# Performance work log

Hardware: AMD Instinct MI355X
Metric: run time of the kernel (lower is better)

The kernel has to match this reference:

```python
import jax, jax.numpy as jnp
import numpy as np

ID, IH, IW = 8, 16, 16
HEADS, DIM_HEAD = 8, 32
INP, OUP = 256, 256
B = 4
N = ID * IH * IW  # 2048
INNER = HEADS * DIM_HEAD  # 256
SCALE = DIM_HEAD ** -0.5


def _make_relative_pos():
    # Faithful to the torch ctor: 3D coords, pairwise diffs, linearize, shift to >=0
    z, y, x = np.meshgrid(np.arange(ID), np.arange(IH), np.arange(IW), indexing='ij')
    coords = np.stack([z.ravel(), y.ravel(), x.ravel()], axis=1)  # [N,3]
    rel = coords[:, None, :] - coords[None, :, :]                 # [N,N,3]
    rp = rel[:, :, 0] * (IH * IW) + rel[:, :, 1] * IW + rel[:, :, 2]
    rp = rp - rp.min()
    return jnp.asarray(rp, dtype=jnp.int32)                       # [N,N]


def setup_inputs() -> dict:
    key = jax.random.key(0)
    k1, k2, k3, k4, k5 = jax.random.split(key, 5)
    table_size = ID * IH * IW * 8  # 16384, as in nn.Embedding ctor
    return {
        "x": jax.random.normal(k1, (B, N, INP), dtype=jnp.float32),
        "w_qkv": jax.random.normal(k2, (INP, 3 * INNER), dtype=jnp.float32) * (INP ** -0.5),
        "bias_table": jax.random.normal(k3, (table_size, 1), dtype=jnp.float32),
        "w_out": jax.random.normal(k4, (INNER, OUP), dtype=jnp.float32) * (INNER ** -0.5),
        "b_out": jax.random.normal(k5, (OUP,), dtype=jnp.float32),
        "relative_pos": _make_relative_pos(),
    }


def reference(x, w_qkv, bias_table, w_out, b_out, relative_pos):
    Bb, Nn, C = x.shape
    qkv = x @ w_qkv                                   # [B, N, 3*H*D]
    qkv = qkv.reshape(Bb, Nn, 3, HEADS, DIM_HEAD)
    qkv = jnp.transpose(qkv, (2, 0, 3, 1, 4))         # [3, B, H, N, D]
    q, k, v = qkv[0], qkv[1], qkv[2]
    q = q * SCALE
    attn = jnp.einsum('bhnd,bhmd->bhnm', q, k)        # [B, H, N, N]
    bias = bias_table[relative_pos, 0]                # [N, N], shared across B,H
    attn = attn + bias
    attn = jax.nn.softmax(attn, axis=-1)
    out = jnp.einsum('bhnm,bhmd->bhnd', attn, v)      # [B, H, N, D]
    out = jnp.transpose(out, (0, 2, 1, 3)).reshape(Bb, Nn, INNER)
    return out @ w_out + b_out                        # dropout p=0 -> identity
```

## Files before the change

kernel.cpp:

```cpp
#include <hip/hip_runtime.h>

typedef unsigned short u16;
typedef unsigned int u32;
typedef __attribute__((ext_vector_type(8))) short bf16x8;
typedef __attribute__((ext_vector_type(4))) float f32x4;

#define MFMA16(a, b, c) __builtin_amdgcn_mfma_f32_16x16x32_bf16(a, b, c, 0, 0, 0)

__device__ __forceinline__ u16 f2bf(float f) {
    union { float f; u32 i; } v; v.f = f;
    u32 x = v.i;
    return (u16)((x + 0x7FFFu + ((x >> 16) & 1u)) >> 16);
}
__device__ __forceinline__ bf16x8 cvt8(const float* __restrict__ p) {
    float4 a = *(const float4*)p;
    float4 b = *(const float4*)(p + 4);
    bf16x8 r;
    r[0] = (short)f2bf(a.x); r[1] = (short)f2bf(a.y);
    r[2] = (short)f2bf(a.z); r[3] = (short)f2bf(a.w);
    r[4] = (short)f2bf(b.x); r[5] = (short)f2bf(b.y);
    r[6] = (short)f2bf(b.z); r[7] = (short)f2bf(b.w);
    return r;
}

__global__ __launch_bounds__(256) void k_transpose(const float* __restrict__ wqkv,
                                                   const float* __restrict__ wout,
                                                   u16* __restrict__ wqkvT,
                                                   u16* __restrict__ woutT) {
    int idx = blockIdx.x * 256 + threadIdx.x;
    if (idx < 768 * 256) {
        int n = idx >> 8, k = idx & 255;
        wqkvT[idx] = f2bf(wqkv[k * 768 + n]);
    }
    if (idx < 256 * 256) {
        int n = idx >> 8, k = idx & 255;
        woutT[idx] = f2bf(wout[k * 256 + n]);
    }
}

__global__ __launch_bounds__(256) void k_gemm_qkv(const float* __restrict__ x,
                                                  const u16* __restrict__ wT,
                                                  u16* __restrict__ qkv) {
    const int tid = threadIdx.x;
    const int wave = tid >> 6, lane = tid & 63, quad = lane >> 4, ql = lane & 15;
    const int mbase = blockIdx.x * 128 + (wave & 1) * 64;
    const int nbase = blockIdx.y * 64 + (wave >> 1) * 32;
    const float QSCALE = 0.17677669529663687f;
    f32x4 acc[4][2];
#pragma unroll
    for (int i = 0; i < 4; ++i)
#pragma unroll
        for (int j = 0; j < 2; ++j) acc[i][j] = (f32x4){0.f, 0.f, 0.f, 0.f};
#pragma unroll
    for (int ks = 0; ks < 8; ++ks) {
        bf16x8 af[4], bfm[2];
#pragma unroll
        for (int ms = 0; ms < 4; ++ms)
            af[ms] = cvt8(x + (size_t)(mbase + ms * 16 + ql) * 256 + ks * 32 + quad * 8);
#pragma unroll
        for (int ns = 0; ns < 2; ++ns)
            bfm[ns] = *(const bf16x8*)(wT + (size_t)(nbase + ns * 16 + ql) * 256 + ks * 32 + quad * 8);
#pragma unroll
        for (int ms = 0; ms < 4; ++ms)
#pragma unroll
            for (int ns = 0; ns < 2; ++ns)
                acc[ms][ns] = MFMA16(af[ms], bfm[ns], acc[ms][ns]);
    }
#pragma unroll
    for (int ms = 0; ms < 4; ++ms)
#pragma unroll
        for (int ns = 0; ns < 2; ++ns) {
            int colb = nbase + ns * 16;
            int t = colb >> 8;
            int Mrow0 = mbase + ms * 16 + quad * 4;
            int bb = Mrow0 >> 11, nn0 = Mrow0 & 2047;
            int col = colb + ql;
            int h = (col & 255) >> 5, d = col & 31;
            if (t == 2) {
                u16 e0 = f2bf(acc[ms][ns][0]), e1 = f2bf(acc[ms][ns][1]);
                u16 e2 = f2bf(acc[ms][ns][2]), e3 = f2bf(acc[ms][ns][3]);
                uint2 pp; pp.x = e0 | ((u32)e1 << 16); pp.y = e2 | ((u32)e3 << 16);
                *(uint2*)(qkv + (size_t)2 * 2097152 + (size_t)(bb * 8 + h) * 65536 +
                          (size_t)d * 2048 + nn0) = pp;
            } else {
                float sc = (t == 0) ? QSCALE : 1.0f;
#pragma unroll
                for (int r = 0; r < 4; ++r)
                    qkv[(size_t)t * 2097152 + ((size_t)(bb * 8 + h) * 2048 + nn0 + r) * 32 + d] =
                        f2bf(acc[ms][ns][r] * sc);
            }
        }
}

__global__ __launch_bounds__(256) void k_attn(const u16* __restrict__ q,
                                              const u16* __restrict__ k,
                                              const u16* __restrict__ vT,
                                              const float* __restrict__ table,
                                              u16* __restrict__ att) {
    __shared__ float tblf[4096];
    __shared__ u32 pT[4][1280];
    const int tid = threadIdx.x;
    const int bh = blockIdx.x & 31, qt = blockIdx.x >> 5;
    const int wave = tid >> 6, lane = tid & 63, quad = lane >> 4, ql = lane & 15;

    for (int i = tid; i < 1024; i += 256)
        ((float4*)tblf)[i] = ((const float4*)table)[i];
    __syncthreads();

    const u16* kbh = k + (size_t)bh * 65536;
    const u16* vbh = vT + (size_t)bh * 65536;
    const int qr0 = qt * 128 + wave * 32 + ql;
    bf16x8 qf[2];
    qf[0] = *(const bf16x8*)(q + ((size_t)bh * 2048 + qr0) * 32 + quad * 8);
    qf[1] = *(const bf16x8*)(q + ((size_t)bh * 2048 + qr0 + 16) * 32 + quad * 8);
    const int base0 = qr0 + 2047 - quad * 4;

    f32x4 oT[2][2], lacc[2];
#pragma unroll
    for (int a = 0; a < 2; ++a) {
        lacc[a] = (f32x4){0.f, 0.f, 0.f, 0.f};
#pragma unroll
        for (int b = 0; b < 2; ++b) oT[a][b] = (f32x4){0.f, 0.f, 0.f, 0.f};
    }
    u32* pw = &pT[wave][0];

#define LOADK(KF, VF, KT) do {                                                          \
    _Pragma("unroll") for (int j_ = 0; j_ < 4; ++j_)                                    \
        KF[j_] = *(const bf16x8*)(kbh + (size_t)((KT) * 64 + j_ * 16 + ql) * 32 + quad * 8); \
    _Pragma("unroll") for (int f_ = 0; f_ < 4; ++f_) {                                  \
        int c_ = f_ >> 1, dt_ = f_ & 1;                                                 \
        VF[f_] = *(const bf16x8*)(vbh + (size_t)(dt_ * 16 + ql) * 2048 +                \
                                  (KT) * 64 + c_ * 32 + quad * 8); }                    \
} while (0)

#define BODY(KF, VF, KT) do {                                                           \
    _Pragma("unroll") for (int qh = 0; qh < 2; ++qh) {                                  \
        f32x4 z_ = {0.f, 0.f, 0.f, 0.f};                                                \
        f32x4 s_[4];                                                                    \
        _Pragma("unroll") for (int j_ = 0; j_ < 4; ++j_)                                \
            s_[j_] = MFMA16(KF[j_], qf[qh], z_);                                        \
        _Pragma("unroll") for (int j_ = 0; j_ < 4; ++j_) {                              \
            _Pragma("unroll") for (int r_ = 0; r_ < 4; ++r_) {                          \
                float sv_ = s_[j_][r_] +                                                \
                    tblf[base0 + qh * 16 - (KT) * 64 - j_ * 16 - r_];                   \
                s_[j_][r_] = __expf(sv_);                                               \
            }                                                                           \
            lacc[qh] += s_[j_];                                                         \
        }                                                                               \
        _Pragma("unroll") for (int j_ = 0; j_ < 4; ++j_)                                \
            _Pragma("unroll") for (int p_ = 0; p_ < 2; ++p_) {                          \
                u32 lo_ = __float_as_uint(s_[j_][2 * p_]) >> 16;                        \
                u32 hi_ = __float_as_uint(s_[j_][2 * p_ + 1]) & 0xFFFF0000u;            \
                pw[(qh * 32 + j_ * 8 + quad * 2 + p_) * 20 + ql] = hi_ | lo_;           \
            }                                                                           \
        _Pragma("unroll") for (int c_ = 0; c_ < 2; ++c_) {                              \
            union { u32 u[4]; bf16x8 v; } bb_;                                          \
            _Pragma("unroll") for (int kk_ = 0; kk_ < 4; ++kk_)                         \
                bb_.u[kk_] = pw[(qh * 32 + c_ * 16 + quad * 4 + kk_) * 20 + ql];        \
            oT[qh][0] = MFMA16(VF[c_ * 2 + 0], bb_.v, oT[qh][0]);                       \
            oT[qh][1] = MFMA16(VF[c_ * 2 + 1], bb_.v, oT[qh][1]);                       \
        }                                                                               \
    }                                                                                   \
} while (0)

    bf16x8 kf0[4], vf0[4], kf1[4], vf1[4];
    LOADK(kf0, vf0, 0);
    for (int kt2 = 0; kt2 < 16; ++kt2) {
        int ktA = 2 * kt2, ktB = 2 * kt2 + 1;
        int ktC = (kt2 == 15) ? 31 : (2 * kt2 + 2);
        LOADK(kf1, vf1, ktB);
        BODY(kf0, vf0, ktA);
        LOADK(kf0, vf0, ktC);
        BODY(kf1, vf1, ktB);
    }
#undef LOADK
#undef BODY

#pragma unroll
    for (int qh = 0; qh < 2; ++qh) {
        float l = lacc[qh][0] + lacc[qh][1] + lacc[qh][2] + lacc[qh][3];
        l += __shfl_xor(l, 16);
        l += __shfl_xor(l, 32);
        float inv = 1.0f / l;
        size_t base = ((size_t)bh * 2048 + qr0 + qh * 16) * 32;
#pragma unroll
        for (int dt = 0; dt < 2; ++dt) {
            u16 e0 = f2bf(oT[qh][dt][0] * inv), e1 = f2bf(oT[qh][dt][1] * inv);
            u16 e2 = f2bf(oT[qh][dt][2] * inv), e3 = f2bf(oT[qh][dt][3] * inv);
            uint2 pp; pp.x = e0 | ((u32)e1 << 16); pp.y = e2 | ((u32)e3 << 16);
            *(uint2*)(att + base + dt * 16 + quad * 4) = pp;
        }
    }
}

__global__ __launch_bounds__(256) void k_gemm_out(const u16* __restrict__ attq,
                                                  const u16* __restrict__ wT,
                                                  const float* __restrict__ bout,
                                                  float* __restrict__ out) {
    const int tid = threadIdx.x;
    const int wave = tid >> 6, lane = tid & 63, quad = lane >> 4, ql = lane & 15;
    const int mbase = blockIdx.x * 128 + (wave & 1) * 64;
    const int nbase = blockIdx.y * 64 + (wave >> 1) * 32;
    f32x4 acc[4][2];
#pragma unroll
    for (int i = 0; i < 4; ++i)
#pragma unroll
        for (int j = 0; j < 2; ++j) acc[i][j] = (f32x4){0.f, 0.f, 0.f, 0.f};
#pragma unroll
    for (int ks = 0; ks < 8; ++ks) {
        bf16x8 af[4], bfm[2];
#pragma unroll
        for (int ms = 0; ms < 4; ++ms) {
            int row = mbase + ms * 16 + ql;
            af[ms] = *(const bf16x8*)(attq +
                ((size_t)((row >> 11) * 8 + ks) * 2048 + (row & 2047)) * 32 + quad * 8);
        }
#pragma unroll
        for (int ns = 0; ns < 2; ++ns)
            bfm[ns] = *(const bf16x8*)(wT + (size_t)(nbase + ns * 16 + ql) * 256 + ks * 32 + quad * 8);
#pragma unroll
        for (int ms = 0; ms < 4; ++ms)
#pragma unroll
            for (int ns = 0; ns < 2; ++ns)
                acc[ms][ns] = MFMA16(af[ms], bfm[ns], acc[ms][ns]);
    }
#pragma unroll
    for (int ms = 0; ms < 4; ++ms)
#pragma unroll
        for (int ns = 0; ns < 2; ++ns)
#pragma unroll
            for (int r = 0; r < 4; ++r) {
                int Mrow = mbase + ms * 16 + quad * 4 + r;
                int col = nbase + ns * 16 + ql;
                out[(size_t)Mrow * 256 + col] = acc[ms][ns][r] + bout[col];
            }
}

extern "C" void kernel_launch(void* const* d_in, const int* in_sizes, int n_in,
                              void* d_out, int out_size, void* d_ws, size_t ws_size,
                              hipStream_t stream) {
    const float* x    = (const float*)d_in[0];
    const float* wqkv = (const float*)d_in[1];
    const float* btab = (const float*)d_in[2];
    const float* wout = (const float*)d_in[3];
    const float* bout = (const float*)d_in[4];
    float* out = (float*)d_out;

    if (ws_size < (size_t)13107200) return;
    u16* ws = (u16*)d_ws;
    u16* wqkvT = ws;
    u16* woutT = wqkvT + 196608;
    u16* qkv   = woutT + 65536;

    hipLaunchKernelGGL(k_transpose, dim3(768), dim3(256), 0, stream, wqkv, wout, wqkvT, woutT);
    hipLaunchKernelGGL(k_gemm_qkv, dim3(64, 12), dim3(256), 0, stream, x, wqkvT, qkv);
    hipLaunchKernelGGL(k_attn, dim3(512), dim3(256), 0, stream,
                       qkv, qkv + 2097152, qkv + 2 * 2097152, btab, qkv);
    hipLaunchKernelGGL(k_gemm_out, dim3(64, 4), dim3(256), 0, stream, qkv, woutT, bout, out);
}
```

Measured before the change: 164.3 us.

## Prep bf16 inputs, fold log2e into scale, shrink attention tiles, MFMA row sums

A single prep kernel now converts x to bf16 (staged in the output buffer) and transposes both weights, folding scale*log2e into the Q weight columns. The QKV GEMM therefore reads bf16 directly and skips per-element scaling. Attention tiles are halved to 64 queries per block (1024 blocks), giving each wave one 16-row Q tile. Each block loads only the slice of the bias table it needs, pre-multiplied by log2e, and uses hardware exp2. Row sums come from an MFMA against a ones vector instead of VALU accumulation and shuffles, and bf16 packing uses a perm instruction. The trade-off is that K/V loads are amortized over fewer queries.

```diff
diff --git a/kernel.cpp b/kernel.cpp
--- a/kernel.cpp
+++ b/kernel.cpp
@@ -7,45 +7,51 @@
 
 #define MFMA16(a, b, c) __builtin_amdgcn_mfma_f32_16x16x32_bf16(a, b, c, 0, 0, 0)
 
+__device__ __forceinline__ float hw_exp2(float x) { return __builtin_amdgcn_exp2f(x); }
+
 __device__ __forceinline__ u16 f2bf(float f) {
     union { float f; u32 i; } v; v.f = f;
     u32 x = v.i;
     return (u16)((x + 0x7FFFu + ((x >> 16) & 1u)) >> 16);
 }
-__device__ __forceinline__ bf16x8 cvt8(const float* __restrict__ p) {
-    float4 a = *(const float4*)p;
-    float4 b = *(const float4*)(p + 4);
-    bf16x8 r;
-    r[0] = (short)f2bf(a.x); r[1] = (short)f2bf(a.y);
-    r[2] = (short)f2bf(a.z); r[3] = (short)f2bf(a.w);
-    r[4] = (short)f2bf(b.x); r[5] = (short)f2bf(b.y);
-    r[6] = (short)f2bf(b.z); r[7] = (short)f2bf(b.w);
-    return r;
-}
-
-__global__ __launch_bounds__(256) void k_transpose(const float* __restrict__ wqkv,
-                                                   const float* __restrict__ wout,
-                                                   u16* __restrict__ wqkvT,
-                                                   u16* __restrict__ woutT) {
-    int idx = blockIdx.x * 256 + threadIdx.x;
-    if (idx < 768 * 256) {
-        int n = idx >> 8, k = idx & 255;
-        wqkvT[idx] = f2bf(wqkv[k * 768 + n]);
-    }
-    if (idx < 256 * 256) {
-        int n = idx >> 8, k = idx & 255;
-        woutT[idx] = f2bf(wout[k * 256 + n]);
-    }
-}
-
-__global__ __launch_bounds__(256) void k_gemm_qkv(const float* __restrict__ x,
+
+__global__ __launch_bounds__(256) void k_prep(const float* __restrict__ x,
+                                              const float* __restrict__ wqkv,
+                                              const float* __restrict__ wout,
+                                              u16* __restrict__ xb,
+                                              u16* __restrict__ wqkvT,
+                                              u16* __restrict__ woutT) {
+    const float QSCALE2 = 0.2550566756538019f;
+    int bx = blockIdx.x, tid = threadIdx.x;
+    if (bx < 1024) {
+        int base = bx * 2048 + tid * 8;
+        float4 a = *(const float4*)(x + base);
+        float4 b = *(const float4*)(x + base + 4);
+        uint4 r;
+        r.x = f2bf(a.x) | ((u32)f2bf(a.y) << 16);
+        r.y = f2bf(a.z) | ((u32)f2bf(a.w) << 16);
+        r.z = f2bf(b.x) | ((u32)f2bf(b.y) << 16);
+        r.w = f2bf(b.z) | ((u32)f2bf(b.w) << 16);
+        *(uint4*)(xb + base) = r;
+    } else if (bx < 1792) {
+        int idx = (bx - 1024) * 256 + tid;
+        int n = idx >> 8, kk = idx & 255;
+        float sc = (n < 256) ? QSCALE2 : 1.0f;
+        wqkvT[idx] = f2bf(wqkv[kk * 768 + n] * sc);
+    } else {
+        int idx = (bx - 1792) * 256 + tid;
+        int n = idx >> 8, kk = idx & 255;
+        woutT[idx] = f2bf(wout[kk * 256 + n]);
+    }
+}
+
+__global__ __launch_bounds__(256) void k_gemm_qkv(const u16* __restrict__ xb,
                                                   const u16* __restrict__ wT,
                                                   u16* __restrict__ qkv) {
     const int tid = threadIdx.x;
     const int wave = tid >> 6, lane = tid & 63, quad = lane >> 4, ql = lane & 15;
     const int mbase = blockIdx.x * 128 + (wave & 1) * 64;
     const int nbase = blockIdx.y * 64 + (wave >> 1) * 32;
-    const float QSCALE = 0.17677669529663687f;
     f32x4 acc[4][2];
 #pragma unroll
     for (int i = 0; i < 4; ++i)
@@ -56,7 +62,7 @@
         bf16x8 af[4], bfm[2];
 #pragma unroll
         for (int ms = 0; ms < 4; ++ms)
-            af[ms] = cvt8(x + (size_t)(mbase + ms * 16 + ql) * 256 + ks * 32 + quad * 8);
+            af[ms] = *(const bf16x8*)(xb + (size_t)(mbase + ms * 16 + ql) * 256 + ks * 32 + quad * 8);
 #pragma unroll
         for (int ns = 0; ns < 2; ++ns)
             bfm[ns] = *(const bf16x8*)(wT + (size_t)(nbase + ns * 16 + ql) * 256 + ks * 32 + quad * 8);
@@ -83,11 +89,10 @@
                 *(uint2*)(qkv + (size_t)2 * 2097152 + (size_t)(bb * 8 + h) * 65536 +
                           (size_t)d * 2048 + nn0) = pp;
             } else {
-                float sc = (t == 0) ? QSCALE : 1.0f;
 #pragma unroll
                 for (int r = 0; r < 4; ++r)
                     qkv[(size_t)t * 2097152 + ((size_t)(bb * 8 + h) * 2048 + nn0 + r) * 32 + d] =
-                        f2bf(acc[ms][ns][r] * sc);
+                        f2bf(acc[ms][ns][r]);
             }
         }
 }
@@ -97,31 +102,32 @@
                                               const u16* __restrict__ vT,
                                               const float* __restrict__ table,
                                               u16* __restrict__ att) {
-    __shared__ float tblf[4096];
-    __shared__ u32 pT[4][1280];
+    __shared__ float tbl2[2112];
+    __shared__ u32 pT[4][640];
     const int tid = threadIdx.x;
     const int bh = blockIdx.x & 31, qt = blockIdx.x >> 5;
     const int wave = tid >> 6, lane = tid & 63, quad = lane >> 4, ql = lane & 15;
-
-    for (int i = tid; i < 1024; i += 256)
-        ((float4*)tblf)[i] = ((const float4*)table)[i];
+    const float LOG2E = 1.4426950408889634f;
+
+    const float4* tg = (const float4*)(table + qt * 64);
+    for (int i = tid; i < 528; i += 256) {
+        float4 t = tg[i];
+        t.x *= LOG2E; t.y *= LOG2E; t.z *= LOG2E; t.w *= LOG2E;
+        ((float4*)tbl2)[i] = t;
+    }
     __syncthreads();
 
     const u16* kbh = k + (size_t)bh * 65536;
     const u16* vbh = vT + (size_t)bh * 65536;
-    const int qr0 = qt * 128 + wave * 32 + ql;
-    bf16x8 qf[2];
-    qf[0] = *(const bf16x8*)(q + ((size_t)bh * 2048 + qr0) * 32 + quad * 8);
-    qf[1] = *(const bf16x8*)(q + ((size_t)bh * 2048 + qr0 + 16) * 32 + quad * 8);
-    const int base0 = qr0 + 2047 - quad * 4;
-
-    f32x4 oT[2][2], lacc[2];
-#pragma unroll
-    for (int a = 0; a < 2; ++a) {
-        lacc[a] = (f32x4){0.f, 0.f, 0.f, 0.f};
-#pragma unroll
-        for (int b = 0; b < 2; ++b) oT[a][b] = (f32x4){0.f, 0.f, 0.f, 0.f};
-    }
+    const int qr0 = qt * 64 + wave * 16 + ql;
+    const bf16x8 qf = *(const bf16x8*)(q + ((size_t)bh * 2048 + qr0) * 32 + quad * 8);
+    const int bloc = wave * 16 + ql + 2047 - quad * 4;
+
+    bf16x8 ones;
+#pragma unroll
+    for (int i = 0; i < 8; ++i) ones[i] = (short)0x3F80;
+
+    f32x4 oT0 = {0.f, 0.f, 0.f, 0.f}, oT1 = {0.f, 0.f, 0.f, 0.f}, oL = {0.f, 0.f, 0.f, 0.f};
     u32* pw = &pT[wave][0];
 
 #define LOADK(KF, VF, KT) do {                                                          \
@@ -134,62 +140,53 @@
 } while (0)
 
 #define BODY(KF, VF, KT) do {                                                           \
-    _Pragma("unroll") for (int qh = 0; qh < 2; ++qh) {                                  \
-        f32x4 z_ = {0.f, 0.f, 0.f, 0.f};                                                \
-        f32x4 s_[4];                                                                    \
-        _Pragma("unroll") for (int j_ = 0; j_ < 4; ++j_)                                \
-            s_[j_] = MFMA16(KF[j_], qf[qh], z_);                                        \
-        _Pragma("unroll") for (int j_ = 0; j_ < 4; ++j_) {                              \
-            _Pragma("unroll") for (int r_ = 0; r_ < 4; ++r_) {                          \
-                float sv_ = s_[j_][r_] +                                                \
-                    tblf[base0 + qh * 16 - (KT) * 64 - j_ * 16 - r_];                   \
-                s_[j_][r_] = __expf(sv_);                                               \
-            }                                                                           \
-            lacc[qh] += s_[j_];                                                         \
-        }                                                                               \
-        _Pragma("unroll") for (int j_ = 0; j_ < 4; ++j_)                                \
-            _Pragma("unroll") for (int p_ = 0; p_ < 2; ++p_) {                          \
-                u32 lo_ = __float_as_uint(s_[j_][2 * p_]) >> 16;                        \
-                u32 hi_ = __float_as_uint(s_[j_][2 * p_ + 1]) & 0xFFFF0000u;            \
-                pw[(qh * 32 + j_ * 8 + quad * 2 + p_) * 20 + ql] = hi_ | lo_;           \
-            }                                                                           \
-        _Pragma("unroll") for (int c_ = 0; c_ < 2; ++c_) {                              \
-            union { u32 u[4]; bf16x8 v; } bb_;                                          \
-            _Pragma("unroll") for (int kk_ = 0; kk_ < 4; ++kk_)                         \
-                bb_.u[kk_] = pw[(qh * 32 + c_ * 16 + quad * 4 + kk_) * 20 + ql];        \
-            oT[qh][0] = MFMA16(VF[c_ * 2 + 0], bb_.v, oT[qh][0]);                       \
-            oT[qh][1] = MFMA16(VF[c_ * 2 + 1], bb_.v, oT[qh][1]);                       \
-        }                                                                               \
+    f32x4 z_ = {0.f, 0.f, 0.f, 0.f};                                                    \
+    f32x4 s_[4];                                                                        \
+    _Pragma("unroll") for (int j_ = 0; j_ < 4; ++j_)                                    \
+        s_[j_] = MFMA16(KF[j_], qf, z_);                                                \
+    _Pragma("unroll") for (int j_ = 0; j_ < 4; ++j_)                                    \
+        _Pragma("unroll") for (int r_ = 0; r_ < 4; ++r_)                                \
+            s_[j_][r_] = hw_exp2(s_[j_][r_] + tbl2[bloc - (KT) * 64 - j_ * 16 - r_]);   \
+    _Pragma("unroll") for (int j_ = 0; j_ < 4; ++j_)                                    \
+        _Pragma("unroll") for (int p_ = 0; p_ < 2; ++p_)                                \
+            pw[(j_ * 8 + quad * 2 + p_) * 20 + ql] = __builtin_amdgcn_perm(             \
+                __float_as_uint(s_[j_][2 * p_ + 1]), __float_as_uint(s_[j_][2 * p_]),   \
+                0x07060302u);                                                           \
+    _Pragma("unroll") for (int c_ = 0; c_ < 2; ++c_) {                                  \
+        union { u32 u[4]; bf16x8 v; } bb_;                                              \
+        _Pragma("unroll") for (int kk_ = 0; kk_ < 4; ++kk_)                             \
+            bb_.u[kk_] = pw[(c_ * 16 + quad * 4 + kk_) * 20 + ql];                      \
+        oT0 = MFMA16(VF[c_ * 2 + 0], bb_.v, oT0);                                      \
+        oT1 = MFMA16(VF[c_ * 2 + 1], bb_.v, oT1);                                      \
+        oL  = MFMA16(ones, bb_.v, oL);                                                  \
     }                                                                                   \
 } while (0)
 
     bf16x8 kf0[4], vf0[4], kf1[4], vf1[4];
     LOADK(kf0, vf0, 0);
     for (int kt2 = 0; kt2 < 16; ++kt2) {
-        int ktA = 2 * kt2, ktB = 2 * kt2 + 1;
+        int ktB = 2 * kt2 + 1;
         int ktC = (kt2 == 15) ? 31 : (2 * kt2 + 2);
         LOADK(kf1, vf1, ktB);
-        BODY(kf0, vf0, ktA);
+        BODY(kf0, vf0, 2 * kt2);
         LOADK(kf0, vf0, ktC);
         BODY(kf1, vf1, ktB);
     }
 #undef LOADK
 #undef BODY
 
-#pragma unroll
-    for (int qh = 0; qh < 2; ++qh) {
-        float l = lacc[qh][0] + lacc[qh][1] + lacc[qh][2] + lacc[qh][3];
-        l += __shfl_xor(l, 16);
-        l += __shfl_xor(l, 32);
-        float inv = 1.0f / l;
-        size_t base = ((size_t)bh * 2048 + qr0 + qh * 16) * 32;
-#pragma unroll
-        for (int dt = 0; dt < 2; ++dt) {
-            u16 e0 = f2bf(oT[qh][dt][0] * inv), e1 = f2bf(oT[qh][dt][1] * inv);
-            u16 e2 = f2bf(oT[qh][dt][2] * inv), e3 = f2bf(oT[qh][dt][3] * inv);
-            uint2 pp; pp.x = e0 | ((u32)e1 << 16); pp.y = e2 | ((u32)e3 << 16);
-            *(uint2*)(att + base + dt * 16 + quad * 4) = pp;
+    float inv = 1.0f / oL[0];
+    size_t base = ((size_t)bh * 2048 + qr0) * 32;
+#pragma unroll
+    for (int dt = 0; dt < 2; ++dt) {
+        u16 e0 = f2bf(oT0[0] * inv), e1 = f2bf(oT0[1] * inv);
+        u16 e2 = f2bf(oT0[2] * inv), e3 = f2bf(oT0[3] * inv);
+        if (dt == 1) {
+            e0 = f2bf(oT1[0] * inv); e1 = f2bf(oT1[1] * inv);
+            e2 = f2bf(oT1[2] * inv); e3 = f2bf(oT1[3] * inv);
         }
+        uint2 pp; pp.x = e0 | ((u32)e1 << 16); pp.y = e2 | ((u32)e3 << 16);
+        *(uint2*)(att + base + dt * 16 + quad * 4) = pp;
     }
 }
 
@@ -251,10 +248,11 @@
     u16* wqkvT = ws;
     u16* woutT = wqkvT + 196608;
     u16* qkv   = woutT + 65536;
-
-    hipLaunchKernelGGL(k_transpose, dim3(768), dim3(256), 0, stream, wqkv, wout, wqkvT, woutT);
-    hipLaunchKernelGGL(k_gemm_qkv, dim3(64, 12), dim3(256), 0, stream, x, wqkvT, qkv);
-    hipLaunchKernelGGL(k_attn, dim3(512), dim3(256), 0, stream,
+    u16* xb    = (u16*)d_out;
+
+    hipLaunchKernelGGL(k_prep, dim3(2048), dim3(256), 0, stream, x, wqkv, wout, xb, wqkvT, woutT);
+    hipLaunchKernelGGL(k_gemm_qkv, dim3(64, 12), dim3(256), 0, stream, xb, wqkvT, qkv);
+    hipLaunchKernelGGL(k_attn, dim3(1024), dim3(256), 0, stream,
                        qkv, qkv + 2097152, qkv + 2 * 2097152, btab, qkv);
     hipLaunchKernelGGL(k_gemm_out, dim3(64, 4), dim3(256), 0, stream, qkv, woutT, bout, out);
 }
```

Result: slower. 194.9 us (+18.7%).
